# Kernel optimization log

Hardware: AMD Instinct MI355X
Metric: run time of the kernel (lower is better)

Reference implementation:

```python
import jax, jax.numpy as jnp
import numpy as np

B, S = 2, 1024
IN, OUT = 1024, 1024
N_IN, N_OUT = 32, 32          # isqrt(IN), isqrt(OUT)
CD = 64                       # compressed_feature_dim
K = 2                         # num_monarchs
D1 = N_IN * N_IN * N_OUT      # 32768, flat M1 size per token
D2 = N_OUT * N_IN * N_OUT     # 32768, flat M2 size per token


def setup_inputs() -> dict:
    key = jax.random.key(0)
    ks = jax.random.split(key, 13)
    g = lambda k, shape, s=0.02: jax.random.normal(k, shape, dtype=jnp.float32) * s
    return {
        "x":  jax.random.normal(ks[0], (B, S, IN), dtype=jnp.float32),
        "Wc": g(ks[1], (IN, CD)),  "bc": g(ks[2], (CD,)),
        "W1": g(ks[3], (K, CD, D1)), "b1": g(ks[4], (K, D1)),
        "W2": g(ks[5], (K, CD, D2)), "b2": g(ks[6], (K, D2)),
        "Wm": g(ks[7], (CD, K)),   "bm": g(ks[8], (K,)),
        "Wb": g(ks[9], (CD, OUT)), "bb": g(ks[10], (OUT,)),
        "Wr": g(ks[11], (CD, 1)),  "br": g(ks[12], (1,)),
    }


def reference(x, Wc, bc, W1, b1, W2, b2, Wm, bm, Wb, bb, Wr, br):
    b, s, _ = x.shape
    # compressor: Linear + Tanh -> [B,S,CD]
    cf = jnp.tanh(x @ Wc + bc)
    # per-expert generated flat weights: [B,S,K,D]
    gen1 = jnp.einsum('bsc,kcd->bskd', cf, W1) + b1
    gen2 = jnp.einsum('bsc,kcd->bskd', cf, W2) + b2
    # expert mixing coefficients -> softmax over K
    coeffs = jax.nn.softmax(cf @ Wm + bm, axis=-1)  # [B,S,K]
    M1f = jnp.einsum('bskd,bsk->bsd', gen1, coeffs)
    M2f = jnp.einsum('bskd,bsk->bsd', gen2, coeffs)
    # Monarch block matmul with per-token weights
    M1 = M1f.reshape(b, s, N_IN, N_IN, N_OUT)   # g=N_IN blocks of [N_IN,N_OUT]
    M2 = M2f.reshape(b, s, N_OUT, N_IN, N_OUT)  # g=N_OUT blocks of [N_IN,N_OUT]
    x1 = x.reshape(b, s, N_IN, N_IN)
    h1 = jnp.einsum('bsgi,bsgio->bsgo', x1, M1)      # [B,S,N_IN,N_OUT]
    h1t = jnp.swapaxes(h1, -1, -2)                   # [B,S,N_OUT,N_IN]
    h2 = jnp.einsum('bsgi,bsgio->bsgo', h1t, M2)     # [B,S,N_OUT,N_OUT]
    y = h2.reshape(b, s, OUT)
    # per-token scale and bias
    ratio = cf @ Wr + br                             # [B,S,1]
    bias = cf @ Wb + bb                              # [B,S,OUT]
    return y * ratio + bias
```

## Files before the change

### kernel.cpp

```cpp
#include <hip/hip_runtime.h>
#include <cstddef>

typedef unsigned short ushortT;
typedef short s8v __attribute__((ext_vector_type(8)));
typedef float f32x4 __attribute__((ext_vector_type(4)));

constexpr int NTOK = 2048;

__device__ inline ushortT f2bf(float f) {
  unsigned u = __float_as_uint(f);
  u += 0x7fffu + ((u >> 16) & 1u);
  return (ushortT)(u >> 16);
}

__device__ inline void gl_lds16(const s8v* g, s8v* l) {
  __builtin_amdgcn_global_load_lds(
      (const __attribute__((address_space(1))) unsigned int*)g,
      (__attribute__((address_space(3))) unsigned int*)l, 16, 0, 0);
}

__device__ inline void pack_slab(
    ushortT (*lds)[1024], int tid, int fac, int g, int jc8,
    const float* __restrict__ W, const float* __restrict__ bv,
    const float* __restrict__ Wb, const float* __restrict__ bb,
    ushortT* __restrict__ P)
{
  const int c4 = tid;
#pragma unroll
  for (int rl = 0; rl < 8; ++rl) {
    int jj = jc8 * 8 + rl;
    float4 v = make_float4(0.f, 0.f, 0.f, 0.f);
    if (fac < 2) {
      if (jj < 128)       v = *(const float4*)(W  + (size_t)jj * 32768 + g * 1024 + c4 * 4);
      else if (jj < 130)  v = *(const float4*)(bv + (size_t)(jj - 128) * 32768 + g * 1024 + c4 * 4);
    } else {
      if (jj < 128)       v = *(const float4*)(Wb + (size_t)(jj & 63) * 1024 + c4 * 4);
      else if (jj < 130)  v = *(const float4*)(bb + c4 * 4);
    }
    int col0 = c4 * 4;
    int sw = col0 ^ ((col0 >> 4) & 0x1C);
    ushortT* d = &lds[rl][sw];
    d[0] = f2bf(v.x); d[1] = f2bf(v.y); d[2] = f2bf(v.z); d[3] = f2bf(v.w);
  }
  __syncthreads();
  const int ks = jc8 >> 2, kkg = jc8 & 3;
#pragma unroll
  for (int it = 0; it < 4; ++it) {
    int idx = tid + it * 256;
    int ct_l = idx >> 4, cl = idx & 15;
    int scol;
    if (fac < 2) {
      int o = ct_l >> 1, ib = (ct_l & 1) * 16;
      scol = (ib + cl) * 32 + o;
    } else {
      scol = ct_l * 16 + cl;
    }
    scol ^= ((scol >> 4) & 0x1C);
    ushortT v[8];
#pragma unroll
    for (int e = 0; e < 8; ++e) v[e] = lds[e][scol];
    size_t ctile = (fac < 2) ? (size_t)(g * 64 + ct_l) : (size_t)ct_l;
    size_t off = ctile * 2560 + (size_t)ks * 512 + (kkg * 16 + cl) * 8;
    uint4 qv;
    qv.x = v[0] | ((unsigned)v[1] << 16);
    qv.y = v[2] | ((unsigned)v[3] << 16);
    qv.z = v[4] | ((unsigned)v[5] << 16);
    qv.w = v[6] | ((unsigned)v[7] << 16);
    *(uint4*)(P + off) = qv;
  }
}

__global__ __launch_bounds__(256) void setup_kernel(
    const float* __restrict__ x, const float* __restrict__ Wc, const float* __restrict__ bc,
    const float* __restrict__ Wm, const float* __restrict__ bm,
    const float* __restrict__ Wr, const float* __restrict__ br,
    const float* __restrict__ W1, const float* __restrict__ b1,
    ushortT* __restrict__ FP, float* __restrict__ ratio, ushortT* __restrict__ P1)
{
  __shared__ __align__(16) char smem[16384];
  const int tid = threadIdx.x;
  const int bid = blockIdx.x;

  if (bid < 512) {
    float* part = (float*)smem;
    float* cf_s = part + 1024;
    float* a0s  = cf_s + 256;
    float* a1s  = a0s + 4;
    const int c = tid & 63;
    const int q = tid >> 6;
    const int t0 = bid * 4;

    float acc[4];
#pragma unroll
    for (int p = 0; p < 4; ++p) acc[p] = 0.f;
    const float* xq = x + (size_t)t0 * 1024 + q * 256;
    const float* wq = Wc + (size_t)(q * 256) * 64 + c;
#pragma unroll 4
    for (int jj = 0; jj < 64; ++jj) {
      float w0 = wq[(jj * 4 + 0) * 64];
      float w1 = wq[(jj * 4 + 1) * 64];
      float w2 = wq[(jj * 4 + 2) * 64];
      float w3 = wq[(jj * 4 + 3) * 64];
#pragma unroll
      for (int p = 0; p < 4; ++p) {
        float4 xv = *(const float4*)(xq + (size_t)p * 1024 + jj * 4);
        acc[p] = fmaf(xv.x, w0, acc[p]);
        acc[p] = fmaf(xv.y, w1, acc[p]);
        acc[p] = fmaf(xv.z, w2, acc[p]);
        acc[p] = fmaf(xv.w, w3, acc[p]);
      }
    }
#pragma unroll
    for (int p = 0; p < 4; ++p) part[(q * 4 + p) * 64 + c] = acc[p];
    __syncthreads();

    {
      int p = tid >> 6, cc = tid & 63;
      float s = part[(0 + p) * 64 + cc] + part[(4 + p) * 64 + cc] +
                part[(8 + p) * 64 + cc] + part[(12 + p) * 64 + cc] + bc[cc];
      cf_s[p * 64 + cc] = tanhf(s);
    }
    __syncthreads();

    {
      float cf = cf_s[q * 64 + c];
      float z0 = cf * Wm[2 * c], z1 = cf * Wm[2 * c + 1], rr = cf * Wr[c];
      for (int off = 32; off; off >>= 1) {
        z0 += __shfl_down(z0, off);
        z1 += __shfl_down(z1, off);
        rr += __shfl_down(rr, off);
      }
      if (c == 0) {
        z0 += bm[0]; z1 += bm[1];
        float mx = fmaxf(z0, z1);
        float e0 = expf(z0 - mx), e1 = expf(z1 - mx);
        float a0 = e0 / (e0 + e1);
        a0s[q] = a0;
        a1s[q] = 1.0f - a0;
        ratio[t0 + q] = rr + br[0];
      }
    }
    __syncthreads();

    const int ks0 = c >> 5, kk = c & 31;
    const int slot = (kk >> 3) * 16, e = kk & 7;
    {
      int t = t0 + q, tt = t >> 4, tok = t & 15;
      size_t base = (size_t)tt * 2560;
      float cf = cf_s[q * 64 + c];
      float a0 = a0s[q], a1 = a1s[q];
      FP[base + (size_t)ks0 * 512 + (slot + tok) * 8 + e]       = f2bf(a0 * cf);
      FP[base + (size_t)(2 + ks0) * 512 + (slot + tok) * 8 + e] = f2bf(a1 * cf);
      if (c < 32) {
        float v = (c == 0) ? a0 : (c == 1) ? a1 : 0.0f;
        FP[base + 4 * 512 + ((c >> 3) * 16 + tok) * 8 + (c & 7)] = f2bf(v);
      }
    }
  } else {
    ushortT (*lds)[1024] = (ushortT (*)[1024])smem;
    int pb = bid - 512;
    pack_slab(lds, tid, 0, pb / 20, pb % 20, W1, b1, nullptr, nullptr, P1);
  }
}

template <int PASS>
__global__ __launch_bounds__(256, 2) void mm_kernel(
    const s8v* __restrict__ fP, const s8v* __restrict__ wP,
    const s8v* __restrict__ wbP,
    const float* __restrict__ xg,
    const float* __restrict__ rat,
    float* __restrict__ outp,
    const float* __restrict__ W2, const float* __restrict__ b2,
    const float* __restrict__ Wb, const float* __restrict__ bb,
    ushortT* __restrict__ P2, ushortT* __restrict__ WbPo)
{
  __shared__ s8v bsh[2][1280];
  __shared__ float xsf[PASS == 1 ? 2112 : 2048];
  __shared__ float hs[PASS == 2 ? 64 : 1][8];
  __shared__ float bls[PASS == 2 ? 64 : 1][8];
  const int tid = threadIdx.x;
  const int bid = blockIdx.x;

  if constexpr (PASS == 1) {
    if (bid >= 512) {
      ushortT (*lds)[1024] = (ushortT (*)[1024])&bsh[0][0];
      int pb = bid - 512;
      if (pb < 640) pack_slab(lds, tid, 1, pb / 20, pb % 20, W2, b2, nullptr, nullptr, P2);
      else          pack_slab(lds, tid, 2, 0, pb - 640, nullptr, nullptr, Wb, bb, WbPo);
      return;
    }
  }

  const int lane = tid & 63;
  const int w = tid >> 6;
  const int cb  = (bid & 7) * 16 + (bid >> 5);
  const int tbgh = (bid >> 3) & 3;
  const int g = cb >> 2;

  const s8v* ap = wP + (size_t)(cb * 16 + w * 4) * 320 + lane;
  s8v a[4][5];
#pragma unroll
  for (int i = 0; i < 4; ++i)
#pragma unroll
    for (int ks = 0; ks < 5; ++ks) a[i][ks] = ap[i * 320 + ks * 64];

  s8v ab[5];
  if constexpr (PASS == 2) {
    const s8v* abp = wbP + (size_t)(cb >> 1) * 320 + lane;
#pragma unroll
    for (int ks = 0; ks < 5; ++ks) ab[ks] = abp[ks * 64];
  }

  const s8v* fbase = fP + (size_t)(tbgh * 8) * 1280;

#pragma unroll
  for (int c2 = 0; c2 < 5; ++c2)
    gl_lds16(fbase + w * 320 + c2 * 64 + lane, &bsh[0][w * 320 + c2 * 64]);
  __syncthreads();

#pragma unroll 1
  for (int tt2 = 0; tt2 < 8; ++tt2) {
    const int buf = tt2 & 1;
    const int t0 = (tbgh * 8 + tt2) * 64;

    float4 xv[2];
#pragma unroll
    for (int it = 0; it < 2; ++it) {
      int idx = tid + it * 256;
      if (PASS == 1) {
        int t = idx >> 3, i4 = idx & 7;
        xv[it] = *(const float4*)(xg + (size_t)(t0 + t) * 1024 + g * 32 + i4 * 4);
      } else {
        int i = idx >> 4, tq = idx & 15;
        xv[it] = *(const float4*)(xg + (size_t)(i * 32 + g) * 2048 + t0 + tq * 4);
      }
    }
    if (tt2 < 7) {
      const s8v* fn = fbase + (size_t)(tt2 + 1) * 1280;
#pragma unroll
      for (int c2 = 0; c2 < 5; ++c2)
        gl_lds16(fn + w * 320 + c2 * 64 + lane, &bsh[buf ^ 1][w * 320 + c2 * 64]);
    }

    f32x4 acc[4][4];
#pragma unroll
    for (int i = 0; i < 4; ++i)
#pragma unroll
      for (int j = 0; j < 4; ++j) acc[i][j] = {0.f, 0.f, 0.f, 0.f};
    f32x4 accb = {0.f, 0.f, 0.f, 0.f};

    __builtin_amdgcn_s_setprio(1);
#pragma unroll
    for (int ks = 0; ks < 5; ++ks) {
      s8v b0 = bsh[buf][0 * 320 + ks * 64 + lane];
      s8v b1 = bsh[buf][1 * 320 + ks * 64 + lane];
      s8v b2v = bsh[buf][2 * 320 + ks * 64 + lane];
      s8v b3 = bsh[buf][3 * 320 + ks * 64 + lane];
      if constexpr (PASS == 2) {
        s8v bw = bsh[buf][w * 320 + ks * 64 + lane];
        accb = __builtin_amdgcn_mfma_f32_16x16x32_bf16(ab[ks], bw, accb, 0, 0, 0);
      }
#pragma unroll
      for (int i = 0; i < 4; ++i) {
        acc[i][0] = __builtin_amdgcn_mfma_f32_16x16x32_bf16(a[i][ks], b0,  acc[i][0], 0, 0, 0);
        acc[i][1] = __builtin_amdgcn_mfma_f32_16x16x32_bf16(a[i][ks], b1,  acc[i][1], 0, 0, 0);
        acc[i][2] = __builtin_amdgcn_mfma_f32_16x16x32_bf16(a[i][ks], b2v, acc[i][2], 0, 0, 0);
        acc[i][3] = __builtin_amdgcn_mfma_f32_16x16x32_bf16(a[i][ks], b3,  acc[i][3], 0, 0, 0);
      }
    }
    __builtin_amdgcn_s_setprio(0);

#pragma unroll
    for (int it = 0; it < 2; ++it) {
      int idx = tid + it * 256;
      float* d;
      if (PASS == 1) { int t = idx >> 3, i4 = idx & 7; d = &xsf[t * 33 + i4 * 4]; }
      else           { int i = idx >> 4, tq = idx & 15; d = &xsf[i * 64 + tq * 4]; }
      d[0] = xv[it].x; d[1] = xv[it].y; d[2] = xv[it].z; d[3] = xv[it].w;
    }
    __syncthreads();

    const int tau = lane & 15, q = lane >> 4;
#pragma unroll
    for (int tt = 0; tt < 4; ++tt) {
      int tl = tt * 16 + tau;
#pragma unroll
      for (int run = 0; run < 2; ++run) {
        float sacc = 0.f;
#pragma unroll
        for (int ch = 0; ch < 2; ++ch) {
          int ct = run * 2 + ch;
          f32x4 av = acc[ct][tt];
#pragma unroll
          for (int r = 0; r < 4; ++r) {
            int i = ch * 16 + q * 4 + r;
            float xvv = (PASS == 1) ? xsf[tl * 33 + i] : xsf[i * 64 + tl];
            sacc = fmaf(av[r], xvv, sacc);
          }
        }
        sacc += __shfl_xor(sacc, 16);
        sacc += __shfl_xor(sacc, 32);
        if constexpr (PASS == 1) {
          if (lane < 16) {
            int colg = g * 32 + (cb & 3) * 8 + w * 2 + run;
            outp[(size_t)colg * 2048 + t0 + tt * 16 + tau] = sacc;
          }
        } else {
          if (lane < 16) hs[tl][w * 2 + run] = sacc;
        }
      }
    }
    if constexpr (PASS == 2) {
      if ((lane >> 5) == (cb & 1)) {
        int ol = ((lane >> 4) & 1) * 4;
#pragma unroll
        for (int r = 0; r < 4; ++r) bls[w * 16 + tau][ol + r] = accb[r];
      }
      __syncthreads();
      if (tid < 128) {
        int row = tid >> 1, half = tid & 1;
        int t = t0 + row;
        int col = g * 32 + (cb & 3) * 8 + half * 4;
        float r = rat[t];
        float4 o;
        o.x = fmaf(hs[row][half * 4 + 0], r, bls[row][half * 4 + 0]);
        o.y = fmaf(hs[row][half * 4 + 1], r, bls[row][half * 4 + 1]);
        o.z = fmaf(hs[row][half * 4 + 2], r, bls[row][half * 4 + 2]);
        o.w = fmaf(hs[row][half * 4 + 3], r, bls[row][half * 4 + 3]);
        *(float4*)(outp + (size_t)t * 1024 + col) = o;
      }
    } else {
      __syncthreads();
    }
  }
}

extern "C" void kernel_launch(void* const* d_in, const int* in_sizes, int n_in,
                              void* d_out, int out_size, void* d_ws, size_t ws_size,
                              hipStream_t stream) {
  const float* x  = (const float*)d_in[0];
  const float* Wc = (const float*)d_in[1];
  const float* bc = (const float*)d_in[2];
  const float* W1 = (const float*)d_in[3];
  const float* b1 = (const float*)d_in[4];
  const float* W2 = (const float*)d_in[5];
  const float* b2 = (const float*)d_in[6];
  const float* Wm = (const float*)d_in[7];
  const float* bm = (const float*)d_in[8];
  const float* Wb = (const float*)d_in[9];
  const float* bb = (const float*)d_in[10];
  const float* Wr = (const float*)d_in[11];
  const float* br = (const float*)d_in[12];
  float* out = (float*)d_out;

  ushortT* P1  = (ushortT*)d_ws;
  ushortT* P2  = P1 + (size_t)2048 * 2560;
  ushortT* WbP = P2 + (size_t)2048 * 2560;
  ushortT* FP  = WbP + (size_t)64 * 2560;
  float* ratio = (float*)(FP + (size_t)128 * 2560);
  float* h1T   = ratio + NTOK;

  setup_kernel<<<dim3(1152), dim3(256), 0, stream>>>(
      x, Wc, bc, Wm, bm, Wr, br, W1, b1, FP, ratio, P1);
  mm_kernel<1><<<dim3(1172), dim3(256), 0, stream>>>(
      (const s8v*)FP, (const s8v*)P1, (const s8v*)WbP, x, nullptr, h1T,
      W2, b2, Wb, bb, P2, WbP);
  mm_kernel<2><<<dim3(512), dim3(256), 0, stream>>>(
      (const s8v*)FP, (const s8v*)P2, (const s8v*)WbP, h1T, ratio, out,
      nullptr, nullptr, nullptr, nullptr, nullptr, nullptr);
}
```

Before: 77.97 us.

## Fuse three kernels into one persistent kernel with grid barriers

```diff
diff --git a/kernel.cpp b/kernel.cpp
--- a/kernel.cpp
+++ b/kernel.cpp
@@ -17,6 +17,17 @@
   __builtin_amdgcn_global_load_lds(
       (const __attribute__((address_space(1))) unsigned int*)g,
       (__attribute__((address_space(3))) unsigned int*)l, 16, 0, 0);
+}
+
+__device__ inline void grid_barrier(unsigned* cnt, unsigned target, int tid) {
+  __syncthreads();
+  if (tid == 0) {
+    __threadfence();
+    atomicAdd(cnt, 1u);
+    while (atomicAdd(cnt, 0u) < target) __builtin_amdgcn_s_sleep(2);
+  }
+  __syncthreads();
+  __threadfence();
 }
 
 __device__ inline void pack_slab(
@@ -70,126 +81,19 @@
   }
 }
 
-__global__ __launch_bounds__(256) void setup_kernel(
-    const float* __restrict__ x, const float* __restrict__ Wc, const float* __restrict__ bc,
-    const float* __restrict__ Wm, const float* __restrict__ bm,
-    const float* __restrict__ Wr, const float* __restrict__ br,
-    const float* __restrict__ W1, const float* __restrict__ b1,
-    ushortT* __restrict__ FP, float* __restrict__ ratio, ushortT* __restrict__ P1)
-{
-  __shared__ __align__(16) char smem[16384];
-  const int tid = threadIdx.x;
-  const int bid = blockIdx.x;
-
-  if (bid < 512) {
-    float* part = (float*)smem;
-    float* cf_s = part + 1024;
-    float* a0s  = cf_s + 256;
-    float* a1s  = a0s + 4;
-    const int c = tid & 63;
-    const int q = tid >> 6;
-    const int t0 = bid * 4;
-
-    float acc[4];
-#pragma unroll
-    for (int p = 0; p < 4; ++p) acc[p] = 0.f;
-    const float* xq = x + (size_t)t0 * 1024 + q * 256;
-    const float* wq = Wc + (size_t)(q * 256) * 64 + c;
-#pragma unroll 4
-    for (int jj = 0; jj < 64; ++jj) {
-      float w0 = wq[(jj * 4 + 0) * 64];
-      float w1 = wq[(jj * 4 + 1) * 64];
-      float w2 = wq[(jj * 4 + 2) * 64];
-      float w3 = wq[(jj * 4 + 3) * 64];
-#pragma unroll
-      for (int p = 0; p < 4; ++p) {
-        float4 xv = *(const float4*)(xq + (size_t)p * 1024 + jj * 4);
-        acc[p] = fmaf(xv.x, w0, acc[p]);
-        acc[p] = fmaf(xv.y, w1, acc[p]);
-        acc[p] = fmaf(xv.z, w2, acc[p]);
-        acc[p] = fmaf(xv.w, w3, acc[p]);
-      }
-    }
-#pragma unroll
-    for (int p = 0; p < 4; ++p) part[(q * 4 + p) * 64 + c] = acc[p];
-    __syncthreads();
-
-    {
-      int p = tid >> 6, cc = tid & 63;
-      float s = part[(0 + p) * 64 + cc] + part[(4 + p) * 64 + cc] +
-                part[(8 + p) * 64 + cc] + part[(12 + p) * 64 + cc] + bc[cc];
-      cf_s[p * 64 + cc] = tanhf(s);
-    }
-    __syncthreads();
-
-    {
-      float cf = cf_s[q * 64 + c];
-      float z0 = cf * Wm[2 * c], z1 = cf * Wm[2 * c + 1], rr = cf * Wr[c];
-      for (int off = 32; off; off >>= 1) {
-        z0 += __shfl_down(z0, off);
-        z1 += __shfl_down(z1, off);
-        rr += __shfl_down(rr, off);
-      }
-      if (c == 0) {
-        z0 += bm[0]; z1 += bm[1];
-        float mx = fmaxf(z0, z1);
-        float e0 = expf(z0 - mx), e1 = expf(z1 - mx);
-        float a0 = e0 / (e0 + e1);
-        a0s[q] = a0;
-        a1s[q] = 1.0f - a0;
-        ratio[t0 + q] = rr + br[0];
-      }
-    }
-    __syncthreads();
-
-    const int ks0 = c >> 5, kk = c & 31;
-    const int slot = (kk >> 3) * 16, e = kk & 7;
-    {
-      int t = t0 + q, tt = t >> 4, tok = t & 15;
-      size_t base = (size_t)tt * 2560;
-      float cf = cf_s[q * 64 + c];
-      float a0 = a0s[q], a1 = a1s[q];
-      FP[base + (size_t)ks0 * 512 + (slot + tok) * 8 + e]       = f2bf(a0 * cf);
-      FP[base + (size_t)(2 + ks0) * 512 + (slot + tok) * 8 + e] = f2bf(a1 * cf);
-      if (c < 32) {
-        float v = (c == 0) ? a0 : (c == 1) ? a1 : 0.0f;
-        FP[base + 4 * 512 + ((c >> 3) * 16 + tok) * 8 + (c & 7)] = f2bf(v);
-      }
-    }
-  } else {
-    ushortT (*lds)[1024] = (ushortT (*)[1024])smem;
-    int pb = bid - 512;
-    pack_slab(lds, tid, 0, pb / 20, pb % 20, W1, b1, nullptr, nullptr, P1);
-  }
-}
-
 template <int PASS>
-__global__ __launch_bounds__(256, 2) void mm_kernel(
+__device__ void mm_phase(
+    char* smem, int tid, int bid,
     const s8v* __restrict__ fP, const s8v* __restrict__ wP,
     const s8v* __restrict__ wbP,
     const float* __restrict__ xg,
     const float* __restrict__ rat,
-    float* __restrict__ outp,
-    const float* __restrict__ W2, const float* __restrict__ b2,
-    const float* __restrict__ Wb, const float* __restrict__ bb,
-    ushortT* __restrict__ P2, ushortT* __restrict__ WbPo)
+    float* __restrict__ outp)
 {
-  __shared__ s8v bsh[2][1280];
-  __shared__ float xsf[PASS == 1 ? 2112 : 2048];
-  __shared__ float hs[PASS == 2 ? 64 : 1][8];
-  __shared__ float bls[PASS == 2 ? 64 : 1][8];
-  const int tid = threadIdx.x;
-  const int bid = blockIdx.x;
-
-  if constexpr (PASS == 1) {
-    if (bid >= 512) {
-      ushortT (*lds)[1024] = (ushortT (*)[1024])&bsh[0][0];
-      int pb = bid - 512;
-      if (pb < 640) pack_slab(lds, tid, 1, pb / 20, pb % 20, W2, b2, nullptr, nullptr, P2);
-      else          pack_slab(lds, tid, 2, 0, pb - 640, nullptr, nullptr, Wb, bb, WbPo);
-      return;
-    }
-  }
+  s8v (*bsh)[1280] = (s8v (*)[1280])smem;
+  float* xsf = (float*)(smem + 40960);
+  float (*hs)[8]  = (float (*)[8])(smem + 49408);
+  float (*bls)[8] = (float (*)[8])(smem + 51456);
 
   const int lane = tid & 63;
   const int w = tid >> 6;
@@ -333,6 +237,128 @@
       __syncthreads();
     }
   }
+}
+
+__global__ __launch_bounds__(256, 2) void fused_kernel(
+    const float* __restrict__ x, const float* __restrict__ Wc, const float* __restrict__ bc,
+    const float* __restrict__ Wm, const float* __restrict__ bm,
+    const float* __restrict__ Wr, const float* __restrict__ br,
+    const float* __restrict__ W1, const float* __restrict__ b1,
+    const float* __restrict__ W2, const float* __restrict__ b2,
+    const float* __restrict__ Wb, const float* __restrict__ bb,
+    ushortT* __restrict__ FP, float* __restrict__ ratio,
+    ushortT* __restrict__ P1, ushortT* __restrict__ P2, ushortT* __restrict__ WbP,
+    float* __restrict__ h1T, float* __restrict__ out, unsigned* __restrict__ bar)
+{
+  __shared__ __align__(16) char smem[53504];
+  const int tid = threadIdx.x;
+  const int bid = blockIdx.x;
+
+  {
+    float* part = (float*)smem;
+    float* cf_s = part + 1024;
+    float* a0s  = cf_s + 256;
+    float* a1s  = a0s + 4;
+    const int c = tid & 63;
+    const int q = tid >> 6;
+    const int t0 = bid * 4;
+
+    float acc[4];
+#pragma unroll
+    for (int p = 0; p < 4; ++p) acc[p] = 0.f;
+    const float* xq = x + (size_t)t0 * 1024 + q * 256;
+    const float* wq = Wc + (size_t)(q * 256) * 64 + c;
+#pragma unroll 4
+    for (int jj = 0; jj < 64; ++jj) {
+      float w0 = wq[(jj * 4 + 0) * 64];
+      float w1 = wq[(jj * 4 + 1) * 64];
+      float w2 = wq[(jj * 4 + 2) * 64];
+      float w3 = wq[(jj * 4 + 3) * 64];
+#pragma unroll
+      for (int p = 0; p < 4; ++p) {
+        float4 xv = *(const float4*)(xq + (size_t)p * 1024 + jj * 4);
+        acc[p] = fmaf(xv.x, w0, acc[p]);
+        acc[p] = fmaf(xv.y, w1, acc[p]);
+        acc[p] = fmaf(xv.z, w2, acc[p]);
+        acc[p] = fmaf(xv.w, w3, acc[p]);
+      }
+    }
+#pragma unroll
+    for (int p = 0; p < 4; ++p) part[(q * 4 + p) * 64 + c] = acc[p];
+    __syncthreads();
+
+    {
+      int p = tid >> 6, cc = tid & 63;
+      float s = part[(0 + p) * 64 + cc] + part[(4 + p) * 64 + cc] +
+                part[(8 + p) * 64 + cc] + part[(12 + p) * 64 + cc] + bc[cc];
+      cf_s[p * 64 + cc] = tanhf(s);
+    }
+    __syncthreads();
+
+    {
+      float cf = cf_s[q * 64 + c];
+      float z0 = cf * Wm[2 * c], z1 = cf * Wm[2 * c + 1], rr = cf * Wr[c];
+      for (int off = 32; off; off >>= 1) {
+        z0 += __shfl_down(z0, off);
+        z1 += __shfl_down(z1, off);
+        rr += __shfl_down(rr, off);
+      }
+      if (c == 0) {
+        z0 += bm[0]; z1 += bm[1];
+        float mx = fmaxf(z0, z1);
+        float e0 = expf(z0 - mx), e1 = expf(z1 - mx);
+        float a0 = e0 / (e0 + e1);
+        a0s[q] = a0;
+        a1s[q] = 1.0f - a0;
+        ratio[t0 + q] = rr + br[0];
+      }
+    }
+    __syncthreads();
+
+    const int ks0 = c >> 5, kk = c & 31;
+    const int slot = (kk >> 3) * 16, e = kk & 7;
+    {
+      int t = t0 + q, tt = t >> 4, tok = t & 15;
+      size_t base = (size_t)tt * 2560;
+      float cf = cf_s[q * 64 + c];
+      float a0 = a0s[q], a1 = a1s[q];
+      FP[base + (size_t)ks0 * 512 + (slot + tok) * 8 + e]       = f2bf(a0 * cf);
+      FP[base + (size_t)(2 + ks0) * 512 + (slot + tok) * 8 + e] = f2bf(a1 * cf);
+      if (c < 32) {
+        float v = (c == 0) ? a0 : (c == 1) ? a1 : 0.0f;
+        FP[base + 4 * 512 + ((c >> 3) * 16 + tok) * 8 + (c & 7)] = f2bf(v);
+      }
+    }
+  }
+  __syncthreads();
+
+  {
+    ushortT (*lds)[1024] = (ushortT (*)[1024])smem;
+#pragma unroll 1
+    for (int si = 0; si < 3; ++si) {
+      int s = bid + si * 512;
+      if (s >= 1300) break;
+      int fac, g, jc8;
+      if (s < 640)       { fac = 0; g = s / 20; jc8 = s % 20; }
+      else if (s < 1280) { fac = 1; int r = s - 640; g = r / 20; jc8 = r % 20; }
+      else               { fac = 2; g = 0; jc8 = s - 1280; }
+      const float* W  = (fac == 0) ? W1 : W2;
+      const float* bv = (fac == 0) ? b1 : b2;
+      ushortT* P = (fac == 0) ? P1 : (fac == 1) ? P2 : WbP;
+      pack_slab(lds, tid, fac, g, jc8, W, bv, Wb, bb, P);
+      __syncthreads();
+    }
+  }
+
+  grid_barrier(bar + 0, 512, tid);
+
+  mm_phase<1>(smem, tid, bid, (const s8v*)FP, (const s8v*)P1, (const s8v*)WbP,
+              x, nullptr, h1T);
+
+  grid_barrier(bar + 1, 512, tid);
+
+  mm_phase<2>(smem, tid, bid, (const s8v*)FP, (const s8v*)P2, (const s8v*)WbP,
+              h1T, ratio, out);
 }
 
 extern "C" void kernel_launch(void* const* d_in, const int* in_sizes, int n_in,
@@ -359,13 +385,10 @@
   ushortT* FP  = WbP + (size_t)64 * 2560;
   float* ratio = (float*)(FP + (size_t)128 * 2560);
   float* h1T   = ratio + NTOK;
-
-  setup_kernel<<<dim3(1152), dim3(256), 0, stream>>>(
-      x, Wc, bc, Wm, bm, Wr, br, W1, b1, FP, ratio, P1);
-  mm_kernel<1><<<dim3(1172), dim3(256), 0, stream>>>(
-      (const s8v*)FP, (const s8v*)P1, (const s8v*)WbP, x, nullptr, h1T,
-      W2, b2, Wb, bb, P2, WbP);
-  mm_kernel<2><<<dim3(512), dim3(256), 0, stream>>>(
-      (const s8v*)FP, (const s8v*)P2, (const s8v*)WbP, h1T, ratio, out,
-      nullptr, nullptr, nullptr, nullptr, nullptr, nullptr);
-}
+  unsigned* bar = (unsigned*)(h1T + (size_t)1024 * 2048);
+
+  hipMemsetAsync(bar, 0, 2 * sizeof(unsigned), stream);
+  fused_kernel<<<dim3(512), dim3(256), 0, stream>>>(
+      x, Wc, bc, Wm, bm, Wr, br, W1, b1, W2, b2, Wb, bb,
+      FP, ratio, P1, P2, WbP, h1T, out, bar);
+}
```

Result: slower. 234.8 us (+201.2%).
